# Kernel optimization log

Measured on AMD Instinct MI355X. Metric: run time of the kernel, lower is better.

## Reference

```python
import jax, jax.numpy as jnp
import numpy as np

D_MODEL = 256
D_INNER = 512
D_STATE = 16
DT_RANK = 16
D_CONV = 4
N_LAYERS = 2
EPS = 1e-5
SEQ_LEN = 16384
IN_DIM = 32
OUT_DIM = 1


def _layernorm(x, g, b):
    m = jnp.mean(x, axis=-1, keepdims=True)
    v = jnp.mean((x - m) ** 2, axis=-1, keepdims=True)
    return (x - m) * jax.lax.rsqrt(v + EPS) * g + b


def _rmsnorm(x, w):
    return x * jax.lax.rsqrt(jnp.mean(x * x, axis=-1, keepdims=True) + EPS) * w


def _selective_scan(x, delta, A, B, C, D):
    # x, delta: (B,L,ED); A: (ED,N); B,C: (B,L,N); D: (ED,)
    dA = jnp.exp(delta[..., None] * A)                    # (B,L,ED,N)
    dBx = (delta * x)[..., None] * B[:, :, None, :]       # (B,L,ED,N)

    def comb(l, r):
        al, bl = l
        ar, br = r
        return (al * ar, bl * ar + br)

    _, hs = jax.lax.associative_scan(comb, (dA, dBx), axis=1)  # (B,L,ED,N)
    y = jnp.einsum('blen,bln->ble', hs, C) + x * D
    return y


def _mamba_block(u, rms_w, inW, convW, convB, xpW, dtW, dtB, A_log, Dp, outW):
    h = _rmsnorm(u, rms_w)
    xz = h @ inW                                   # (B,L,2*ED)
    xin, z = jnp.split(xz, 2, axis=-1)
    # depthwise causal conv1d over time
    xc = jax.lax.conv_general_dilated(
        jnp.transpose(xin, (0, 2, 1)), convW,
        window_strides=(1,), padding=[(D_CONV - 1, 0)],
        feature_group_count=D_INNER,
        dimension_numbers=('NCH', 'OIH', 'NCH')) + convB[None, :, None]
    xs = jax.nn.silu(jnp.transpose(xc, (0, 2, 1)))  # (B,L,ED)
    dbc = xs @ xpW                                  # (B,L,dt_rank+2N)
    delta = jax.nn.softplus(dbc[..., :DT_RANK] @ dtW + dtB)
    Bm = dbc[..., DT_RANK:DT_RANK + D_STATE]
    Cm = dbc[..., DT_RANK + D_STATE:]
    y = _selective_scan(xs, delta, -jnp.exp(A_log), Bm, Cm, Dp)
    out = (y * jax.nn.silu(z)) @ outW
    return u + out  # residual


def _forward(x, W_in, b_in, ln1_g, ln1_b,
             rms_w, inW, convW, convB, xpW, dtW, dtB, A_log, Dp, outW,
             ln2_g, ln2_b, W1, b1, ln3_g, ln3_b, W2, b2):
    # input_proj (dropout = identity in eval)
    h = jax.nn.gelu(_layernorm(x[0] @ W_in + b_in, ln1_g, ln1_b))
    h = h[None]  # (1,L,D)
    for i in range(N_LAYERS):
        h = _mamba_block(h, rms_w[i], inW[i], convW[i], convB[i], xpW[i],
                         dtW[i], dtB[i], A_log[i], Dp[i], outW[i])
    # output_proj
    h = _layernorm(h, ln2_g, ln2_b)
    h = jax.nn.gelu(h @ W1 + b1)
    h = _layernorm(h, ln3_g, ln3_b)
    h = jnp.tanh(h @ W2 + b2)
    return h.reshape(-1)


def setup_inputs() -> dict:
    key = jax.random.key(0)
    ks = jax.random.split(key, 16)
    s = 0.02
    A = jnp.tile(jnp.arange(1, D_STATE + 1, dtype=jnp.float32)[None, :], (D_INNER, 1))
    return {
        'x': jax.random.normal(ks[0], (1, SEQ_LEN, IN_DIM), jnp.float32),
        'W_in': s * jax.random.normal(ks[1], (IN_DIM, D_MODEL), jnp.float32),
        'b_in': jnp.zeros((D_MODEL,), jnp.float32),
        'ln1_g': jnp.ones((D_MODEL,), jnp.float32),
        'ln1_b': jnp.zeros((D_MODEL,), jnp.float32),
        'rms_w': jnp.ones((N_LAYERS, D_MODEL), jnp.float32),
        'inW': s * jax.random.normal(ks[2], (N_LAYERS, D_MODEL, 2 * D_INNER), jnp.float32),
        'convW': s * jax.random.normal(ks[3], (N_LAYERS, D_INNER, 1, D_CONV), jnp.float32),
        'convB': jnp.zeros((N_LAYERS, D_INNER), jnp.float32),
        'xpW': s * jax.random.normal(ks[4], (N_LAYERS, D_INNER, DT_RANK + 2 * D_STATE), jnp.float32),
        'dtW': s * jax.random.normal(ks[5], (N_LAYERS, DT_RANK, D_INNER), jnp.float32),
        'dtB': 0.1 * jax.random.normal(ks[6], (N_LAYERS, D_INNER), jnp.float32),
        'A_log': jnp.tile(jnp.log(A)[None], (N_LAYERS, 1, 1)),
        'Dp': jnp.ones((N_LAYERS, D_INNER), jnp.float32),
        'outW': s * jax.random.normal(ks[7], (N_LAYERS, D_INNER, D_MODEL), jnp.float32),
        'ln2_g': jnp.ones((D_MODEL,), jnp.float32),
        'ln2_b': jnp.zeros((D_MODEL,), jnp.float32),
        'W1': s * jax.random.normal(ks[8], (D_MODEL, D_MODEL // 2), jnp.float32),
        'b1': jnp.zeros((D_MODEL // 2,), jnp.float32),
        'ln3_g': jnp.ones((D_MODEL // 2,), jnp.float32),
        'ln3_b': jnp.zeros((D_MODEL // 2,), jnp.float32),
        'W2': s * jax.random.normal(ks[9], (D_MODEL // 2, OUT_DIM), jnp.float32),
        'b2': jnp.zeros((OUT_DIM,), jnp.float32),
    }


def reference(x, W_in, b_in, ln1_g, ln1_b, rms_w, inW, convW, convB, xpW,
              dtW, dtB, A_log, Dp, outW, ln2_g, ln2_b, W1, b1, ln3_g, ln3_b,
              W2, b2):
    return _forward(x, W_in, b_in, ln1_g, ln1_b, rms_w, inW, convW, convB,
                    xpW, dtW, dtB, A_log, Dp, outW, ln2_g, ln2_b, W1, b1,
                    ln3_g, ln3_b, W2, b2)
```

## Files before the change

### kernel.cpp

```cpp
#include <hip/hip_runtime.h>
#include <hip/hip_bf16.h>
#include <math.h>

#define L_SEQ 16384
#define DM 256
#define DI 512
#define DS 16
#define NCH 512
#define CHL 32
#define CLB 16

typedef __attribute__((ext_vector_type(8))) short short8v;
typedef __attribute__((ext_vector_type(4))) float f32x4;

__device__ __forceinline__ float tanh_fast(float x){
  float xc = fminf(x, 15.f);
  float t = __expf(2.f*xc);
  return (t-1.f)/(t+1.f);
}
__device__ __forceinline__ float gelu_f(float x){
  float x3 = x*x*x;
  return 0.5f*x*(1.0f + tanh_fast(0.7978845608028654f*(x + 0.044715f*x3)));
}
__device__ __forceinline__ float silu_f(float x){
  return x / (1.0f + __expf(-x));
}
__device__ __forceinline__ float softplus_f(float x){
  return fmaxf(x,0.0f) + __logf(1.0f + __expf(-fabsf(x)));
}
__device__ __forceinline__ float bf2f(unsigned short u){
  return __uint_as_float(((unsigned int)u)<<16);
}
__device__ __forceinline__ void gload16(const void* g, void* l){
  __builtin_amdgcn_global_load_lds((const __attribute__((address_space(1))) void*)g,
                                   (__attribute__((address_space(3))) void*)l, 16, 0, 0);
}

__device__ __forceinline__ void powers16(float r, float* dA){
  float r2 = r*r;
  float r4 = r2*r2;
  float r8 = r4*r4;
  dA[0]=r;        dA[1]=r2;       dA[2]=r2*r;     dA[3]=r4;
  dA[4]=r4*r;     dA[5]=r4*r2;    dA[6]=r4*dA[2]; dA[7]=r8;
  dA[8]=r8*r;     dA[9]=r8*r2;    dA[10]=r8*dA[2];dA[11]=r8*r4;
  dA[12]=r8*dA[4];dA[13]=r8*dA[5];dA[14]=r8*dA[6];dA[15]=r8*r8;
}

__global__ void k_prep(const float* __restrict__ inW, const float* __restrict__ rmsw,
                       const float* __restrict__ outW, const float* __restrict__ W1,
                       const float* __restrict__ xpW, const float* __restrict__ dtW,
                       __hip_bfloat16* __restrict__ inWt, __hip_bfloat16* __restrict__ outWt,
                       __hip_bfloat16* __restrict__ W1t, __hip_bfloat16* __restrict__ Wdbc_t){
  int idx = blockIdx.x*256 + threadIdx.x;
  if(idx < 524288){
    int layer = idx >> 18;
    int r = idx & 262143;
    int n = r >> 8, k = r & 255;
    inWt[idx] = __float2bfloat16(inW[layer*262144 + k*1024 + n] * rmsw[layer*256+k]);
  } else if(idx < 786432){
    int j = idx - 524288;
    int layer = j >> 17;
    int r = j & 131071;
    int n = r >> 9, k = r & 511;
    outWt[j] = __float2bfloat16(outW[layer*131072 + k*256 + n]);
  } else if(idx < 819200){
    int j = idx - 786432;
    int n = j >> 8, k = j & 255;
    W1t[j] = __float2bfloat16(W1[k*128 + n]);
  } else if(idx < 1474560){
    int j = idx - 819200;
    int layer = j / 327680;
    int r = j % 327680;
    int n = r >> 9, k = r & 511;
    const float* xp = xpW + layer*512*48;
    float v;
    if(n < 512){
      const float* dt = dtW + layer*16*512;
      float s = 0.f;
#pragma unroll
      for(int q=0;q<16;q++) s = fmaf(xp[k*48+q], dt[q*512+n], s);
      v = s;
    } else if(n < 544){
      v = xp[k*48 + 16 + (n-512)];
    } else v = 0.f;
    Wdbc_t[j] = __float2bfloat16(v);
  }
}

__global__ void k_zero(float* __restrict__ p, int n4){
  int i = blockIdx.x*256 + threadIdx.x;
  if(i < n4) ((float4*)p)[i] = make_float4(0.f,0.f,0.f,0.f);
}

__global__ __launch_bounds__(256) void k_input(const float* __restrict__ x,
                        const float* __restrict__ Win, const float* __restrict__ bin,
                        const float* __restrict__ g, const float* __restrict__ b,
                        __hip_bfloat16* __restrict__ u, float* __restrict__ rowsq){
  int wv = threadIdx.x>>6, lane = threadIdx.x&63;
  int r = blockIdx.x*4 + wv;
  int c0 = lane*4;
  float acc[4];
  { float4 bv = *(const float4*)&bin[c0];
    acc[0]=bv.x; acc[1]=bv.y; acc[2]=bv.z; acc[3]=bv.w; }
#pragma unroll
  for(int k=0;k<32;k++){
    float xk = x[r*32+k];
    float4 wv4 = *(const float4*)&Win[k*DM+c0];
    acc[0]=fmaf(xk,wv4.x,acc[0]); acc[1]=fmaf(xk,wv4.y,acc[1]);
    acc[2]=fmaf(xk,wv4.z,acc[2]); acc[3]=fmaf(xk,wv4.w,acc[3]);
  }
  float s = (acc[0]+acc[1])+(acc[2]+acc[3]);
  float sq = acc[0]*acc[0]+acc[1]*acc[1]+acc[2]*acc[2]+acc[3]*acc[3];
#pragma unroll
  for(int o=32;o;o>>=1){ s += __shfl_xor(s,o); sq += __shfl_xor(sq,o); }
  float mean = s*(1.0f/DM);
  float var = sq*(1.0f/DM) - mean*mean;
  float rs = rsqrtf(var+1e-5f);
  float4 gv = *(const float4*)&g[c0];
  float4 bv = *(const float4*)&b[c0];
  float go[4];
  go[0] = gelu_f((acc[0]-mean)*rs*gv.x+bv.x);
  go[1] = gelu_f((acc[1]-mean)*rs*gv.y+bv.y);
  go[2] = gelu_f((acc[2]-mean)*rs*gv.z+bv.z);
  go[3] = gelu_f((acc[3]-mean)*rs*gv.w+bv.w);
  float ssq = go[0]*go[0]+go[1]*go[1]+go[2]*go[2]+go[3]*go[3];
#pragma unroll
  for(int o=32;o;o>>=1) ssq += __shfl_xor(ssq,o);
  if(lane==0) rowsq[r] = ssq;
  __hip_bfloat16 ob[4] = {__float2bfloat16(go[0]),__float2bfloat16(go[1]),
                          __float2bfloat16(go[2]),__float2bfloat16(go[3])};
  *(uint2*)&u[r*DM+c0] = *(uint2*)ob;
}

__global__ __launch_bounds__(256) void k_ln(const __hip_bfloat16* __restrict__ u,
                     const float* __restrict__ g, const float* __restrict__ b,
                     __hip_bfloat16* __restrict__ o){
  int wv = threadIdx.x>>6, lane = threadIdx.x&63;
  int r = blockIdx.x*4 + wv;
  int c0 = lane*4;
  ushort4 uv = *(const ushort4*)&u[r*DM+c0];
  float v[4] = {bf2f(uv.x), bf2f(uv.y), bf2f(uv.z), bf2f(uv.w)};
  float s = (v[0]+v[1])+(v[2]+v[3]);
  float sq = v[0]*v[0]+v[1]*v[1]+v[2]*v[2]+v[3]*v[3];
#pragma unroll
  for(int o2=32;o2;o2>>=1){ s += __shfl_xor(s,o2); sq += __shfl_xor(sq,o2); }
  float mean = s*(1.0f/DM);
  float var = sq*(1.0f/DM) - mean*mean;
  float rs = rsqrtf(var+1e-5f);
  float4 gv = *(const float4*)&g[c0];
  float4 bv = *(const float4*)&b[c0];
  __hip_bfloat16 ob[4] = {
    __float2bfloat16((v[0]-mean)*rs*gv.x+bv.x),
    __float2bfloat16((v[1]-mean)*rs*gv.y+bv.y),
    __float2bfloat16((v[2]-mean)*rs*gv.z+bv.z),
    __float2bfloat16((v[3]-mean)*rs*gv.w+bv.w)};
  *(uint2*)&o[r*DM+c0] = *(uint2*)ob;
}

template<int EPI, typename OT>
__global__ __launch_bounds__(512) void k_mgemm(const __hip_bfloat16* __restrict__ A,
    const __hip_bfloat16* __restrict__ Wt, const float* __restrict__ bias,
    const OT* __restrict__ R, OT* __restrict__ C, float* __restrict__ C2,
    float* __restrict__ rowsq, int M, int K, int ldc, int Nout){
  __shared__ char lds[66560];
  float* Ob = (float*)lds;
  int t = threadIdx.x, lane = t&63, wave = t>>6;
  int gx = gridDim.x;
  int f = blockIdx.y*gx + blockIdx.x;
  int s = f >> 3;
  int sy = s/gx;
  int yb = (f&7)*(gridDim.y>>3) + sy;
  int xb = s - sy*gx;
  int m0 = yb*128, n0 = xb*128;
  int wm = (wave>>1)*32, wn = (wave&1)*64;
  f32x4 acc[2][4] = {};
  int soff[2], srow[2], scol[2];
#pragma unroll
  for(int c=0;c<2;c++){
    int off = c*8192 + t*16;
    int row = off>>7;
    int sl  = ((off>>4)&7) ^ (row&7);
    soff[c]=off; srow[c]=row; scol[c]=sl*8;
  }
  int nk = K >> 6;
#pragma unroll
  for(int c=0;c<2;c++){
    gload16(&A [(m0+srow[c])*K + scol[c]], lds + soff[c]);
    gload16(&Wt[(n0+srow[c])*K + scol[c]], lds + 32768 + soff[c]);
  }
  for(int ki=0; ki<nk; ki++){
    int co = (ki & 1) ? 16384 : 0;
    if(ki+1 < nk){
      int no = co ^ 16384;
      int kt = (ki+1)<<6;
#pragma unroll
      for(int c=0;c<2;c++){
        gload16(&A [(m0+srow[c])*K + kt + scol[c]], lds + no + soff[c]);
        gload16(&Wt[(n0+srow[c])*K + kt + scol[c]], lds + 32768 + no + soff[c]);
      }
      asm volatile("s_waitcnt vmcnt(4)" ::: "memory");
    } else {
      asm volatile("s_waitcnt vmcnt(0)" ::: "memory");
    }
    __builtin_amdgcn_s_barrier();
    asm volatile("" ::: "memory");
    const short* As = (const short*)(lds + co);
    const short* Bs = (const short*)(lds + 32768 + co);
#pragma unroll
    for(int ks=0; ks<2; ks++){
      short8v a[2], b[4];
      int k8 = ks*4 + (lane>>4);
#pragma unroll
      for(int i=0;i<2;i++){
        int lr = wm + i*16 + (lane&15);
        a[i] = *(const short8v*)&As[lr*64 + (k8 ^ (lr&7))*8];
      }
#pragma unroll
      for(int j=0;j<4;j++){
        int lr = wn + j*16 + (lane&15);
        b[j] = *(const short8v*)&Bs[lr*64 + (k8 ^ (lr&7))*8];
      }
#pragma unroll
      for(int i=0;i<2;i++)
#pragma unroll
        for(int j=0;j<4;j++)
          acc[i][j] = __builtin_amdgcn_mfma_f32_16x16x32_bf16(a[i], b[j], acc[i][j], 0,0,0);
    }
    asm volatile("" ::: "memory");
    __builtin_amdgcn_s_barrier();
  }
#pragma unroll
  for(int h=0; h<2; h++){
    __syncthreads();
    if((wm>>6)==h){
      int base = wm & 63;
#pragma unroll
      for(int i=0;i<2;i++)
#pragma unroll
        for(int j=0;j<4;j++)
#pragma unroll
          for(int r=0;r<4;r++)
            Ob[(base + i*16 + (lane>>4)*4 + r)*132 + wn + j*16 + (lane&15)] = acc[i][j][r];
    }
    __syncthreads();
    float ssq_acc = 0.f;
#pragma unroll
    for(int v=0; v<4; v++){
      int fidx = (t*4+v)*4;
      int row = fidx>>7, col = fidx&127;
      if(col < Nout){
        float4 o = *(const float4*)&Ob[row*132 + col];
        int grow = m0 + h*64 + row, gcol = n0 + col;
        if(EPI==1 || EPI==5){
          if constexpr(sizeof(OT)==2){
            ushort4 rv = *(const ushort4*)&R[grow*ldc+gcol];
            o.x+=bf2f(rv.x); o.y+=bf2f(rv.y); o.z+=bf2f(rv.z); o.w+=bf2f(rv.w);
          } else {
            float4 rv = *(const float4*)&R[grow*ldc+gcol];
            o.x+=rv.x; o.y+=rv.y; o.z+=rv.z; o.w+=rv.w;
          }
          if(EPI==5) ssq_acc += o.x*o.x + o.y*o.y + o.z*o.z + o.w*o.w;
        }
        if(EPI==2){
          float4 bv = *(const float4*)&bias[gcol];
          o.x=gelu_f(o.x+bv.x); o.y=gelu_f(o.y+bv.y);
          o.z=gelu_f(o.z+bv.z); o.w=gelu_f(o.w+bv.w);
        }
        if(EPI==6){
          float rs = rsqrtf(rowsq[grow]*(1.0f/DM) + 1e-5f);
          o.x*=rs; o.y*=rs; o.z*=rs; o.w*=rs;
        }
        if(EPI==4){
          if(gcol < 512){
            float4 bv = *(const float4*)&bias[gcol];
            float4 so = {softplus_f(o.x+bv.x), softplus_f(o.y+bv.y),
                         softplus_f(o.z+bv.z), softplus_f(o.w+bv.w)};
            __hip_bfloat16 ob[4] = {__float2bfloat16(so.x),__float2bfloat16(so.y),
                                    __float2bfloat16(so.z),__float2bfloat16(so.w)};
            *(uint2*)&C[grow*ldc+gcol] = *(uint2*)ob;
          } else {
            *(float4*)&C2[grow*32 + (gcol-512)] = o;
          }
        } else {
          if constexpr(sizeof(OT)==2){
            __hip_bfloat16 ob[4] = {__float2bfloat16(o.x),__float2bfloat16(o.y),
                                    __float2bfloat16(o.z),__float2bfloat16(o.w)};
            *(uint2*)&C[grow*ldc+gcol] = *(uint2*)ob;
          } else {
            *(float4*)&C[grow*ldc+gcol] = o;
          }
        }
      }
    }
    if(EPI==5){
      ssq_acc += __shfl_xor(ssq_acc,1);
      ssq_acc += __shfl_xor(ssq_acc,2);
      ssq_acc += __shfl_xor(ssq_acc,4);
      if((t&7)==0) atomicAdd(&rowsq[m0 + h*64 + (t>>3)], ssq_acc);
    }
  }
}

__global__ __launch_bounds__(256) void k_conv(const __hip_bfloat16* __restrict__ xz,
                       const float* __restrict__ cw, const float* __restrict__ cb,
                       __hip_bfloat16* __restrict__ xs_bf){
  int idx = blockIdx.x*256 + threadIdx.x;
  int cg = idx & 127, lb = idx >> 7;
  int c4 = cg*4;
  int l0 = lb*CLB;
  float w[4][4], bias[4];
#pragma unroll
  for(int j=0;j<4;j++){
    float4 wv = *(const float4*)&cw[(c4+j)*4];
    w[j][0]=wv.x; w[j][1]=wv.y; w[j][2]=wv.z; w[j][3]=wv.w;
  }
  { float4 bv = *(const float4*)&cb[c4];
    bias[0]=bv.x; bias[1]=bv.y; bias[2]=bv.z; bias[3]=bv.w; }
  float xm0[4], xm1[4], xm2[4];
#pragma unroll
  for(int j=0;j<4;j++){ xm0[j]=0.f; xm1[j]=0.f; xm2[j]=0.f; }
  if(l0 >= 3){
    ushort4 r0 = *(const ushort4*)&xz[(l0-3)*1024 + c4];
    ushort4 r1 = *(const ushort4*)&xz[(l0-2)*1024 + c4];
    ushort4 r2 = *(const ushort4*)&xz[(l0-1)*1024 + c4];
    xm0[0]=bf2f(r0.x); xm0[1]=bf2f(r0.y); xm0[2]=bf2f(r0.z); xm0[3]=bf2f(r0.w);
    xm1[0]=bf2f(r1.x); xm1[1]=bf2f(r1.y); xm1[2]=bf2f(r1.z); xm1[3]=bf2f(r1.w);
    xm2[0]=bf2f(r2.x); xm2[1]=bf2f(r2.y); xm2[2]=bf2f(r2.z); xm2[3]=bf2f(r2.w);
  }
#pragma unroll 4
  for(int l=l0; l<l0+CLB; l++){
    ushort4 rc = *(const ushort4*)&xz[l*1024 + c4];
    float xc[4] = {bf2f(rc.x), bf2f(rc.y), bf2f(rc.z), bf2f(rc.w)};
    __hip_bfloat16 ob[4];
#pragma unroll
    for(int j=0;j<4;j++){
      float acc = bias[j];
      acc = fmaf(xm0[j], w[j][0], acc);
      acc = fmaf(xm1[j], w[j][1], acc);
      acc = fmaf(xm2[j], w[j][2], acc);
      acc = fmaf(xc[j],  w[j][3], acc);
      ob[j] = __float2bfloat16(silu_f(acc));
    }
    *(uint2*)&xs_bf[l*DI + c4] = *(uint2*)ob;
#pragma unroll
    for(int j=0;j<4;j++){ xm0[j]=xm1[j]; xm1[j]=xm2[j]; xm2[j]=xc[j]; }
  }
}

__global__ __launch_bounds__(256) void k_scan1(const __hip_bfloat16* __restrict__ delta,
                        const __hip_bfloat16* __restrict__ xs,
                        const float* __restrict__ dbc32, const float* __restrict__ A_log,
                        float* __restrict__ Atot, float* __restrict__ Btot){
  __shared__ float bcs[CHL*32];
  int t = threadIdx.x;
  int chunk = blockIdx.x >> 1;
  int e = ((blockIdx.x & 1) << 8) + t;
  int l0 = chunk*CHL;
  ((float4*)bcs)[t] = ((const float4*)&dbc32[l0*32])[t];
  float A[16];
  {
    const float4* al = (const float4*)&A_log[e*DS];
#pragma unroll
    for(int q=0;q<4;q++){
      float4 a = al[q];
      A[q*4+0] = -__expf(a.x); A[q*4+1] = -__expf(a.y);
      A[q*4+2] = -__expf(a.z); A[q*4+3] = -__expf(a.w);
    }
  }
  bool pf = true;
#pragma unroll
  for(int n=1;n<16;n++) pf = pf && (fabsf(A[n] - (n+1)*A[0]) <= 1e-4f*fabsf(A[n]));
  float carry[16], aprod[16];
#pragma unroll
  for(int n=0;n<16;n++){ carry[n]=0.f; aprod[n]=1.f; }
  __syncthreads();
  if(pf){
    float A0 = A[0];
#pragma unroll 2
    for(int li=0; li<CHL; li++){
      int l = l0 + li;
      float d  = bf2f(*(const unsigned short*)&delta[l*DI+e]);
      float xv = bf2f(*(const unsigned short*)&xs[l*DI+e]);
      float dxv = d*xv;
      const float4* bp = (const float4*)&bcs[li*32];
      float4 b0=bp[0], b1=bp[1], b2=bp[2], b3=bp[3];
      float B[16] = {b0.x,b0.y,b0.z,b0.w, b1.x,b1.y,b1.z,b1.w,
                     b2.x,b2.y,b2.z,b2.w, b3.x,b3.y,b3.z,b3.w};
      float r = __expf(d*A0);
      float dA[16]; powers16(r, dA);
#pragma unroll
      for(int n=0;n<16;n++){
        carry[n] = fmaf(carry[n], dA[n], dxv*B[n]);
        aprod[n] *= dA[n];
      }
    }
  } else {
#pragma unroll 2
    for(int li=0; li<CHL; li++){
      int l = l0 + li;
      float d  = bf2f(*(const unsigned short*)&delta[l*DI+e]);
      float xv = bf2f(*(const unsigned short*)&xs[l*DI+e]);
      float dxv = d*xv;
      const float4* bp = (const float4*)&bcs[li*32];
      float4 b0=bp[0], b1=bp[1], b2=bp[2], b3=bp[3];
      float B[16] = {b0.x,b0.y,b0.z,b0.w, b1.x,b1.y,b1.z,b1.w,
                     b2.x,b2.y,b2.z,b2.w, b3.x,b3.y,b3.z,b3.w};
#pragma unroll
      for(int n=0;n<16;n++){
        float dA = __expf(d*A[n]);
        carry[n] = fmaf(carry[n], dA, dxv*B[n]);
        aprod[n] *= dA;
      }
    }
  }
  float4* ap = (float4*)&Atot[chunk*8192 + e*DS];
  float4* bp = (float4*)&Btot[chunk*8192 + e*DS];
#pragma unroll
  for(int q=0;q<4;q++){
    ap[q] = make_float4(aprod[q*4],aprod[q*4+1],aprod[q*4+2],aprod[q*4+3]);
    bp[q] = make_float4(carry[q*4],carry[q*4+1],carry[q*4+2],carry[q*4+3]);
  }
}

__global__ void k_scan2(const float* __restrict__ Atot, const float* __restrict__ Btot,
                        float* __restrict__ h0){
  int tg = blockIdx.x*256 + threadIdx.x;
  float carry = 0.f;
  for(int c0=0;c0<NCH;c0+=8){
    float a[8], b[8];
#pragma unroll
    for(int j=0;j<8;j++){
      a[j] = Atot[(c0+j)*8192+tg];
      b[j] = Btot[(c0+j)*8192+tg];
    }
#pragma unroll
    for(int j=0;j<8;j++){
      h0[(c0+j)*8192+tg] = carry;
      carry = fmaf(carry, a[j], b[j]);
    }
  }
}

__global__ __launch_bounds__(256) void k_scan3(const __hip_bfloat16* __restrict__ delta,
                        const __hip_bfloat16* __restrict__ xs,
                        const float* __restrict__ dbc32, const float* __restrict__ A_log,
                        const float* __restrict__ Dp, const float* __restrict__ h0,
                        const __hip_bfloat16* __restrict__ xz, __hip_bfloat16* __restrict__ y){
  __shared__ float bcs[CHL*32];
  int t = threadIdx.x;
  int chunk = blockIdx.x >> 1;
  int e = ((blockIdx.x & 1) << 8) + t;
  int l0 = chunk*CHL;
  ((float4*)bcs)[t] = ((const float4*)&dbc32[l0*32])[t];
  float A[16];
  {
    const float4* al = (const float4*)&A_log[e*DS];
#pragma unroll
    for(int q=0;q<4;q++){
      float4 a = al[q];
      A[q*4+0] = -__expf(a.x); A[q*4+1] = -__expf(a.y);
      A[q*4+2] = -__expf(a.z); A[q*4+3] = -__expf(a.w);
    }
  }
  bool pf = true;
#pragma unroll
  for(int n=1;n<16;n++) pf = pf && (fabsf(A[n] - (n+1)*A[0]) <= 1e-4f*fabsf(A[n]));
  float carry[16];
  {
    const float4* hp = (const float4*)&h0[chunk*8192 + e*DS];
#pragma unroll
    for(int q=0;q<4;q++){
      float4 h = hp[q];
      carry[q*4+0]=h.x; carry[q*4+1]=h.y; carry[q*4+2]=h.z; carry[q*4+3]=h.w;
    }
  }
  float Dv = Dp[e];
  __syncthreads();
  if(pf){
    float A0 = A[0];
#pragma unroll 2
    for(int li=0; li<CHL; li++){
      int l = l0 + li;
      float d  = bf2f(*(const unsigned short*)&delta[l*DI+e]);
      float xv = bf2f(*(const unsigned short*)&xs[l*DI+e]);
      float dxv = d*xv;
      const float4* bp = (const float4*)&bcs[li*32];
      float4 b0=bp[0], b1=bp[1], b2=bp[2], b3=bp[3];
      float4 c0=bp[4], c1=bp[5], c2=bp[6], c3=bp[7];
      float B[16] = {b0.x,b0.y,b0.z,b0.w, b1.x,b1.y,b1.z,b1.w,
                     b2.x,b2.y,b2.z,b2.w, b3.x,b3.y,b3.z,b3.w};
      float Cv[16] = {c0.x,c0.y,c0.z,c0.w, c1.x,c1.y,c1.z,c1.w,
                      c2.x,c2.y,c2.z,c2.w, c3.x,c3.y,c3.z,c3.w};
      float r = __expf(d*A0);
      float dA[16]; powers16(r, dA);
      float p[4] = {0.f,0.f,0.f,0.f};
#pragma unroll
      for(int n=0;n<16;n++){
        carry[n] = fmaf(carry[n], dA[n], dxv*B[n]);
        p[n&3] = fmaf(carry[n], Cv[n], p[n&3]);
      }
      float ps = (p[0]+p[1]) + (p[2]+p[3]);
      float z = bf2f(*(const unsigned short*)&xz[l*1024 + 512 + e]);
      y[l*DI+e] = __float2bfloat16(fmaf(xv, Dv, ps) * silu_f(z));
    }
  } else {
#pragma unroll 2
    for(int li=0; li<CHL; li++){
      int l = l0 + li;
      float d  = bf2f(*(const unsigned short*)&delta[l*DI+e]);
      float xv = bf2f(*(const unsigned short*)&xs[l*DI+e]);
      float dxv = d*xv;
      const float4* bp = (const float4*)&bcs[li*32];
      float4 b0=bp[0], b1=bp[1], b2=bp[2], b3=bp[3];
      float4 c0=bp[4], c1=bp[5], c2=bp[6], c3=bp[7];
      float B[16] = {b0.x,b0.y,b0.z,b0.w, b1.x,b1.y,b1.z,b1.w,
                     b2.x,b2.y,b2.z,b2.w, b3.x,b3.y,b3.z,b3.w};
      float Cv[16] = {c0.x,c0.y,c0.z,c0.w, c1.x,c1.y,c1.z,c1.w,
                      c2.x,c2.y,c2.z,c2.w, c3.x,c3.y,c3.z,c3.w};
      float p[4] = {0.f,0.f,0.f,0.f};
#pragma unroll
      for(int n=0;n<16;n++){
        float dA = __expf(d*A[n]);
        carry[n] = fmaf(carry[n], dA, dxv*B[n]);
        p[n&3] = fmaf(carry[n], Cv[n], p[n&3]);
      }
      float ps = (p[0]+p[1]) + (p[2]+p[3]);
      float z = bf2f(*(const unsigned short*)&xz[l*1024 + 512 + e]);
      y[l*DI+e] = __float2bfloat16(fmaf(xv, Dv, ps) * silu_f(z));
    }
  }
}

__global__ void k_final(const float* __restrict__ h2, const float* __restrict__ g,
                        const float* __restrict__ b, const float* __restrict__ W2,
                        const float* __restrict__ b2, float* __restrict__ out){
  int lane = threadIdx.x&63;
  int wv = threadIdx.x>>6;
  int r = blockIdx.x*4 + wv;
  float v0 = h2[r*128+lane], v1 = h2[r*128+64+lane];
  float s = v0+v1, sq = v0*v0+v1*v1;
#pragma unroll
  for(int o=32;o;o>>=1){ s += __shfl_xor(s,o); sq += __shfl_xor(sq,o); }
  float mean = s*(1.0f/128), var = sq*(1.0f/128) - mean*mean;
  float rs = rsqrtf(var+1e-5f);
  float n0 = (v0-mean)*rs*g[lane]+b[lane];
  float n1 = (v1-mean)*rs*g[lane+64]+b[lane+64];
  float d = n0*W2[lane] + n1*W2[lane+64];
#pragma unroll
  for(int o=32;o;o>>=1) d += __shfl_xor(d,o);
  if(lane==0) out[r] = tanhf(d + b2[0]);
}

extern "C" void kernel_launch(void* const* d_in, const int* in_sizes, int n_in,
                              void* d_out, int out_size, void* d_ws, size_t ws_size,
                              hipStream_t stream){
  const float* x    = (const float*)d_in[0];
  const float* Win  = (const float*)d_in[1];
  const float* bin  = (const float*)d_in[2];
  const float* ln1g = (const float*)d_in[3];
  const float* ln1b = (const float*)d_in[4];
  const float* rmsw = (const float*)d_in[5];
  const float* inW  = (const float*)d_in[6];
  const float* convW= (const float*)d_in[7];
  const float* convB= (const float*)d_in[8];
  const float* xpW  = (const float*)d_in[9];
  const float* dtW  = (const float*)d_in[10];
  const float* dtB  = (const float*)d_in[11];
  const float* A_log= (const float*)d_in[12];
  const float* Dp   = (const float*)d_in[13];
  const float* outW = (const float*)d_in[14];
  const float* ln2g = (const float*)d_in[15];
  const float* ln2b = (const float*)d_in[16];
  const float* W1   = (const float*)d_in[17];
  const float* b1   = (const float*)d_in[18];
  const float* ln3g = (const float*)d_in[19];
  const float* ln3b = (const float*)d_in[20];
  const float* W2   = (const float*)d_in[21];
  const float* b2   = (const float*)d_in[22];
  float* out = (float*)d_out;
  float* ws = (float*)d_ws;
  __hip_bfloat16* u_bf = (__hip_bfloat16*)ws;
  float* rowsq0 = ws + 4194304;
  float* rowsq1 = ws + 4210688;
  __hip_bfloat16* hn_bf = (__hip_bfloat16*)(ws + 4259840);
  __hip_bfloat16* xz_bf = (__hip_bfloat16*)(ws + 8388608);
  float* dbc32 = ws + 16777216;
  __hip_bfloat16* delta_bf = (__hip_bfloat16*)(ws + 17301504);
  __hip_bfloat16* y_bf  = (__hip_bfloat16*)(ws + 25690112);
  __hip_bfloat16* xs_bf = (__hip_bfloat16*)(ws + 29884416);
  float* Atot  = ws + 34078720;
  float* Btot  = ws + 38273024;
  float* h0    = Btot;
  float* h2    = ws;
  __hip_bfloat16* inWt   = (__hip_bfloat16*)(ws + 42467328);
  __hip_bfloat16* outWt  = (__hip_bfloat16*)(ws + 42729472);
  __hip_bfloat16* W1t    = (__hip_bfloat16*)(ws + 42860544);
  __hip_bfloat16* Wdbc_t = (__hip_bfloat16*)(ws + 42876928);

  k_prep<<<5760,256,0,stream>>>(inW, rmsw, outW, W1, xpW, dtW, inWt, outWt, W1t, Wdbc_t);
  k_zero<<<16,256,0,stream>>>(rowsq1, 16384/4);
  k_input<<<L_SEQ/4,256,0,stream>>>(x,Win,bin,ln1g,ln1b,u_bf,rowsq0);
  for(int i=0;i<2;i++){
    float* rsq_in = (i==0) ? rowsq0 : rowsq1;
    k_mgemm<6,__hip_bfloat16><<<dim3(8, L_SEQ/128),512,0,stream>>>(
        u_bf, inWt+i*262144, nullptr, nullptr, xz_bf, nullptr, rsq_in, L_SEQ, DM, 1024, 1024);
    k_conv<<<(L_SEQ/CLB)*128/256,256,0,stream>>>(xz_bf, convW+i*DI*4, convB+i*DI, xs_bf);
    k_mgemm<4,__hip_bfloat16><<<dim3(5, L_SEQ/128),512,0,stream>>>(
        xs_bf, Wdbc_t+i*327680, dtB+i*DI, nullptr, delta_bf, dbc32, nullptr, L_SEQ, DI, 512, 544);
    k_scan1<<<NCH*2,256,0,stream>>>(delta_bf, xs_bf, dbc32, A_log+i*DI*DS, Atot, Btot);
    k_scan2<<<32,256,0,stream>>>(Atot, Btot, h0);
    k_scan3<<<NCH*2,256,0,stream>>>(delta_bf, xs_bf, dbc32, A_log+i*DI*DS, Dp+i*DI, h0, xz_bf, y_bf);
    if(i==0){
      k_mgemm<5,__hip_bfloat16><<<dim3(2, L_SEQ/128),512,0,stream>>>(
          y_bf, outWt, nullptr, u_bf, u_bf, nullptr, rowsq1, L_SEQ, DI, 256, 256);
    } else {
      k_mgemm<1,__hip_bfloat16><<<dim3(2, L_SEQ/128),512,0,stream>>>(
          y_bf, outWt+131072, nullptr, u_bf, u_bf, nullptr, nullptr, L_SEQ, DI, 256, 256);
    }
  }
  k_ln<<<L_SEQ/4,256,0,stream>>>(u_bf, ln2g, ln2b, hn_bf);
  k_mgemm<2,float><<<dim3(1, L_SEQ/128),512,0,stream>>>(
      hn_bf, W1t, b1, nullptr, h2, nullptr, nullptr, L_SEQ, DM, 128, 128);
  k_final<<<L_SEQ/4,256,0,stream>>>(h2, ln3g, ln3b, W2, b2, out);
}
```

Measured before the change: 373.2 us.

## Store chunk scan carries in bf16, spread scan2 over more blocks, fold zeroing into prep

The per-chunk A-product and B-carry totals and the propagated chunk-start states now live in bf16 instead of fp32, halving the traffic between the three scan phases. The sequential cross-chunk scan launches 128 blocks of 64 threads instead of 32 of 256, spreading the serial pass across more CUs. The separate zeroing kernel is merged into the weight-prep kernel, saving one launch. Rounding carries and states to bf16 reduces accuracy of the recurrence state.

```diff
diff --git a/kernel.cpp b/kernel.cpp
--- a/kernel.cpp
+++ b/kernel.cpp
@@ -50,7 +50,8 @@
                        const float* __restrict__ outW, const float* __restrict__ W1,
                        const float* __restrict__ xpW, const float* __restrict__ dtW,
                        __hip_bfloat16* __restrict__ inWt, __hip_bfloat16* __restrict__ outWt,
-                       __hip_bfloat16* __restrict__ W1t, __hip_bfloat16* __restrict__ Wdbc_t){
+                       __hip_bfloat16* __restrict__ W1t, __hip_bfloat16* __restrict__ Wdbc_t,
+                       float* __restrict__ rowsq1){
   int idx = blockIdx.x*256 + threadIdx.x;
   if(idx < 524288){
     int layer = idx >> 18;
@@ -84,12 +85,9 @@
       v = xp[k*48 + 16 + (n-512)];
     } else v = 0.f;
     Wdbc_t[j] = __float2bfloat16(v);
-  }
-}
-
-__global__ void k_zero(float* __restrict__ p, int n4){
-  int i = blockIdx.x*256 + threadIdx.x;
-  if(i < n4) ((float4*)p)[i] = make_float4(0.f,0.f,0.f,0.f);
+  } else if(idx < 1490944){
+    rowsq1[idx - 1474560] = 0.f;
+  }
 }
 
 __global__ __launch_bounds__(256) void k_input(const float* __restrict__ x,
@@ -350,7 +348,7 @@
 __global__ __launch_bounds__(256) void k_scan1(const __hip_bfloat16* __restrict__ delta,
                         const __hip_bfloat16* __restrict__ xs,
                         const float* __restrict__ dbc32, const float* __restrict__ A_log,
-                        float* __restrict__ Atot, float* __restrict__ Btot){
+                        __hip_bfloat16* __restrict__ Atot, __hip_bfloat16* __restrict__ Btot){
   __shared__ float bcs[CHL*32];
   int t = threadIdx.x;
   int chunk = blockIdx.x >> 1;
@@ -413,29 +411,33 @@
       }
     }
   }
-  float4* ap = (float4*)&Atot[chunk*8192 + e*DS];
-  float4* bp = (float4*)&Btot[chunk*8192 + e*DS];
-#pragma unroll
-  for(int q=0;q<4;q++){
-    ap[q] = make_float4(aprod[q*4],aprod[q*4+1],aprod[q*4+2],aprod[q*4+3]);
-    bp[q] = make_float4(carry[q*4],carry[q*4+1],carry[q*4+2],carry[q*4+3]);
-  }
-}
-
-__global__ void k_scan2(const float* __restrict__ Atot, const float* __restrict__ Btot,
-                        float* __restrict__ h0){
-  int tg = blockIdx.x*256 + threadIdx.x;
+  __hip_bfloat16 apk[16], bpk[16];
+#pragma unroll
+  for(int n=0;n<16;n++){
+    apk[n] = __float2bfloat16(aprod[n]);
+    bpk[n] = __float2bfloat16(carry[n]);
+  }
+  uint4* ap = (uint4*)&Atot[chunk*8192 + e*DS];
+  uint4* bp = (uint4*)&Btot[chunk*8192 + e*DS];
+  ap[0] = ((const uint4*)apk)[0]; ap[1] = ((const uint4*)apk)[1];
+  bp[0] = ((const uint4*)bpk)[0]; bp[1] = ((const uint4*)bpk)[1];
+}
+
+__global__ __launch_bounds__(64) void k_scan2(const __hip_bfloat16* __restrict__ Atot,
+                        const __hip_bfloat16* __restrict__ Btot,
+                        __hip_bfloat16* __restrict__ h0){
+  int tg = blockIdx.x*64 + threadIdx.x;
   float carry = 0.f;
   for(int c0=0;c0<NCH;c0+=8){
     float a[8], b[8];
 #pragma unroll
     for(int j=0;j<8;j++){
-      a[j] = Atot[(c0+j)*8192+tg];
-      b[j] = Btot[(c0+j)*8192+tg];
+      a[j] = bf2f(*(const unsigned short*)&Atot[(c0+j)*8192+tg]);
+      b[j] = bf2f(*(const unsigned short*)&Btot[(c0+j)*8192+tg]);
     }
 #pragma unroll
     for(int j=0;j<8;j++){
-      h0[(c0+j)*8192+tg] = carry;
+      h0[(c0+j)*8192+tg] = __float2bfloat16(carry);
       carry = fmaf(carry, a[j], b[j]);
     }
   }
@@ -444,7 +446,7 @@
 __global__ __launch_bounds__(256) void k_scan3(const __hip_bfloat16* __restrict__ delta,
                         const __hip_bfloat16* __restrict__ xs,
                         const float* __restrict__ dbc32, const float* __restrict__ A_log,
-                        const float* __restrict__ Dp, const float* __restrict__ h0,
+                        const float* __restrict__ Dp, const __hip_bfloat16* __restrict__ h0,
                         const __hip_bfloat16* __restrict__ xz, __hip_bfloat16* __restrict__ y){
   __shared__ float bcs[CHL*32];
   int t = threadIdx.x;
@@ -467,12 +469,14 @@
   for(int n=1;n<16;n++) pf = pf && (fabsf(A[n] - (n+1)*A[0]) <= 1e-4f*fabsf(A[n]));
   float carry[16];
   {
-    const float4* hp = (const float4*)&h0[chunk*8192 + e*DS];
-#pragma unroll
-    for(int q=0;q<4;q++){
-      float4 h = hp[q];
-      carry[q*4+0]=h.x; carry[q*4+1]=h.y; carry[q*4+2]=h.z; carry[q*4+3]=h.w;
-    }
+    uint4 h0a = ((const uint4*)&h0[chunk*8192 + e*DS])[0];
+    uint4 h0b = ((const uint4*)&h0[chunk*8192 + e*DS])[1];
+    const unsigned short* hp = (const unsigned short*)&h0a;
+#pragma unroll
+    for(int n=0;n<8;n++) carry[n] = bf2f(hp[n]);
+    const unsigned short* hq = (const unsigned short*)&h0b;
+#pragma unroll
+    for(int n=0;n<8;n++) carry[8+n] = bf2f(hq[n]);
   }
   float Dv = Dp[e];
   __syncthreads();
@@ -588,17 +592,16 @@
   __hip_bfloat16* delta_bf = (__hip_bfloat16*)(ws + 17301504);
   __hip_bfloat16* y_bf  = (__hip_bfloat16*)(ws + 25690112);
   __hip_bfloat16* xs_bf = (__hip_bfloat16*)(ws + 29884416);
-  float* Atot  = ws + 34078720;
-  float* Btot  = ws + 38273024;
-  float* h0    = Btot;
+  __hip_bfloat16* Atot  = (__hip_bfloat16*)(ws + 34078720);
+  __hip_bfloat16* Btot  = (__hip_bfloat16*)(ws + 36175872);
+  __hip_bfloat16* h0    = Btot;
   float* h2    = ws;
   __hip_bfloat16* inWt   = (__hip_bfloat16*)(ws + 42467328);
   __hip_bfloat16* outWt  = (__hip_bfloat16*)(ws + 42729472);
   __hip_bfloat16* W1t    = (__hip_bfloat16*)(ws + 42860544);
   __hip_bfloat16* Wdbc_t = (__hip_bfloat16*)(ws + 42876928);
 
-  k_prep<<<5760,256,0,stream>>>(inW, rmsw, outW, W1, xpW, dtW, inWt, outWt, W1t, Wdbc_t);
-  k_zero<<<16,256,0,stream>>>(rowsq1, 16384/4);
+  k_prep<<<5824,256,0,stream>>>(inW, rmsw, outW, W1, xpW, dtW, inWt, outWt, W1t, Wdbc_t, rowsq1);
   k_input<<<L_SEQ/4,256,0,stream>>>(x,Win,bin,ln1g,ln1b,u_bf,rowsq0);
   for(int i=0;i<2;i++){
     float* rsq_in = (i==0) ? rowsq0 : rowsq1;
@@ -608,7 +611,7 @@
     k_mgemm<4,__hip_bfloat16><<<dim3(5, L_SEQ/128),512,0,stream>>>(
         xs_bf, Wdbc_t+i*327680, dtB+i*DI, nullptr, delta_bf, dbc32, nullptr, L_SEQ, DI, 512, 544);
     k_scan1<<<NCH*2,256,0,stream>>>(delta_bf, xs_bf, dbc32, A_log+i*DI*DS, Atot, Btot);
-    k_scan2<<<32,256,0,stream>>>(Atot, Btot, h0);
+    k_scan2<<<128,64,0,stream>>>(Atot, Btot, h0);
     k_scan3<<<NCH*2,256,0,stream>>>(delta_bf, xs_bf, dbc32, A_log+i*DI*DS, Dp+i*DI, h0, xz_bf, y_bf);
     if(i==0){
       k_mgemm<5,__hip_bfloat16><<<dim3(2, L_SEQ/128),512,0,stream>>>(
```

New measurement: 357.7 us. 4.1% less time.
